# Kernel tuning notes

Measured on AMD Instinct MI355X. Metric: run time of the kernel, lower is better.

Reference implementation:

```python
import jax, jax.numpy as jnp
import numpy as np

N = 512      # state dim n
K = 8        # num_regimes
H = 256      # hidden dim for g0/g1/gate MLPs
B = 8192     # batch
INIT_SCALE = 0.1


def _mlp(x, w1, b1, w2, b2, w3, b3):
    # 2 hidden SiLU layers + linear head (matches ScalarMLP/GateNet with num_layers=2)
    h = jax.nn.silu(x @ w1 + b1)
    h = jax.nn.silu(h @ w2 + b2)
    return h @ w3 + b3


def setup_inputs() -> dict:
    key = jax.random.key(0)
    ks = jax.random.split(key, 12)

    def lin(k, fi, fo):
        kw, kb = jax.random.split(k)
        s = 1.0 / np.sqrt(fi)  # torch nn.Linear default init range
        w = jax.random.uniform(kw, (fi, fo), minval=-s, maxval=s, dtype=jnp.float32)
        b = jax.random.uniform(kb, (fo,), minval=-s, maxval=s, dtype=jnp.float32)
        return w, b

    g0_w1, g0_b1 = lin(ks[0], N, H)
    g0_w2, g0_b2 = lin(ks[1], H, H)
    g0_w3, g0_b3 = lin(ks[2], H, 1)
    g1_w1, g1_b1 = lin(ks[3], N, H)
    g1_w2, g1_b2 = lin(ks[4], H, H)
    g1_w3, g1_b3 = lin(ks[5], H, 1)
    gt_w1, gt_b1 = lin(ks[6], N, H)
    gt_w2, gt_b2 = lin(ks[7], H, H)
    gt_w3, gt_b3 = lin(ks[8], H, K)
    W = jax.random.uniform(ks[9], (K, N, N), minval=-INIT_SCALE, maxval=INIT_SCALE, dtype=jnp.float32)
    z = jax.random.normal(ks[10], (B, 2 * N), dtype=jnp.float32)
    return dict(z=z,
                g0_w1=g0_w1, g0_b1=g0_b1, g0_w2=g0_w2, g0_b2=g0_b2, g0_w3=g0_w3, g0_b3=g0_b3,
                g1_w1=g1_w1, g1_b1=g1_b1, g1_w2=g1_w2, g1_b2=g1_b2, g1_w3=g1_w3, g1_b3=g1_b3,
                gt_w1=gt_w1, gt_b1=gt_b1, gt_w2=gt_w2, gt_b2=gt_b2, gt_w3=gt_w3, gt_b3=gt_b3,
                W=W)


def reference(z,
              g0_w1, g0_b1, g0_w2, g0_b2, g0_w3, g0_b3,
              g1_w1, g1_b1, g1_w2, g1_b2, g1_w3, g1_b3,
              gt_w1, gt_b1, gt_w2, gt_b2, gt_w3, gt_b3,
              W):
    n = W.shape[-1]
    x0, x1 = z[:, :n], z[:, n:]

    def U(x0_, x1_):
        e0 = jnp.sum(_mlp(x0_, g0_w1, g0_b1, g0_w2, g0_b2, g0_w3, g0_b3))  # scalar
        e1 = jnp.sum(_mlp(x1_, g1_w1, g1_b1, g1_w2, g1_b2, g1_w3, g1_b3))
        alpha = jax.nn.softmax(_mlp(x0_, gt_w1, gt_b1, gt_w2, gt_b2, gt_w3, gt_b3), axis=-1)  # [B,K]
        # per-sample per-regime bilinear x1^T W_k x0 -> avoids materializing [B,n,n] W_eff
        q = jnp.einsum('bi,kij,bj->bk', x1_, W, x0_)
        return e0 + e1 + jnp.sum(alpha * q)

    grad_x0, grad_x1 = jax.grad(U, argnums=(0, 1))(x0, x1)
    return jnp.concatenate([-grad_x0, -grad_x1], axis=-1)  # [B, 2n]
```

## Files before the change

kernel.cpp:

```cpp
#include <hip/hip_runtime.h>
#include <cstdint>
#include <cstddef>

constexpr int BTOT = 8192, N = 512, H = 256, K = 8;

typedef __attribute__((ext_vector_type(8))) short short8v;
typedef __attribute__((ext_vector_type(4))) float f32x4;

__device__ __forceinline__ float bf2f(unsigned short u) {
    return __uint_as_float(((uint32_t)u) << 16);
}
__device__ __forceinline__ unsigned short f2bf(float f) {
    uint32_t u = __float_as_uint(f);
    uint32_t r = (u + 0x7FFFu + ((u >> 16) & 1u)) >> 16;
    return (unsigned short)r;
}

typedef __attribute__((address_space(3))) unsigned int lds_uint;
typedef __attribute__((address_space(1))) const unsigned int glob_uint;
__device__ __forceinline__ void async16(const unsigned short* g, unsigned short* l) {
    __builtin_amdgcn_global_load_lds((glob_uint*)g, (lds_uint*)l, 16, 0, 0);
}

struct GArg {
    const unsigned short* A;
    const unsigned short* Bt;
    const float* bias;
    const float* w3v;
    const unsigned short* dmul;
    unsigned short* ob;
    unsigned short* ob2;
    float* of;
    int lda, ldbt, Ka, lddm, ldob, ldof;
};

enum { EPI_BF = 0, EPI_FWD = 1, EPI_BWD2 = 2, EPI_NEG = 3, EPI_NEGW = 4 };

template<int EPI>
__global__ __launch_bounds__(256) void gemm_g(GArg ga0, GArg ga1, GArg ga2)
{
    const int z = blockIdx.z;
    const GArg g = (z == 0) ? ga0 : (z == 1) ? ga1 : ga2;

    __shared__ __attribute__((aligned(16))) unsigned short As[3 * 128 * 32];
    __shared__ __attribute__((aligned(16))) unsigned short Bs[3 * 128 * 32];
    const int tid = threadIdx.x;
    const int lane = tid & 63, wave = tid >> 6;
    const int m0 = blockIdx.y * 128, n0 = blockIdx.x * 128;
    const int wr = (wave >> 1) * 64, wc = (wave & 1) * 64;
    const int rr = lane & 15;
    const int kb = ((lane >> 4) ^ (lane & 3)) << 3;

    const int r0 = tid >> 2;
    const int ko0 = (((tid & 3) ^ (r0 & 3)) << 3);
    const unsigned short* gA0 = g.A + (size_t)(m0 + r0) * g.lda + ko0;
    const unsigned short* gA1 = g.A + (size_t)(m0 + r0 + 64) * g.lda + ko0;
    const unsigned short* gB0 = g.Bt + (size_t)(n0 + r0) * g.ldbt + ko0;
    const unsigned short* gB1 = g.Bt + (size_t)(n0 + r0 + 64) * g.ldbt + ko0;

    auto stage = [&](int t, int buf) {
        const int k0 = t << 5;
        async16(gA0 + k0, As + buf * 4096 + tid * 8);
        async16(gA1 + k0, As + buf * 4096 + (tid + 256) * 8);
        async16(gB0 + k0, Bs + buf * 4096 + tid * 8);
        async16(gB1 + k0, Bs + buf * 4096 + (tid + 256) * 8);
    };

    f32x4 acc[4][4];
    #pragma unroll
    for (int i = 0; i < 4; ++i)
        #pragma unroll
        for (int j = 0; j < 4; ++j) acc[i][j] = (f32x4){0.f, 0.f, 0.f, 0.f};

    const int nt = g.Ka >> 5;

    stage(0, 0);
    if (nt > 1) stage(1, 1);

    int buf = 0;
    for (int t = 0; t < nt; ++t) {
        if (t + 1 < nt) { asm volatile("s_waitcnt vmcnt(4)" ::: "memory"); }
        else            { asm volatile("s_waitcnt vmcnt(0)" ::: "memory"); }
        __builtin_amdgcn_s_barrier();
        if (t + 2 < nt) {
            int b2 = buf + 2; if (b2 >= 3) b2 -= 3;
            stage(t + 2, b2);
        }
        short8v af[4], bfr[4];
        #pragma unroll
        for (int i = 0; i < 4; ++i)
            af[i] = *(const short8v*)(As + buf * 4096 + (wr + i * 16 + rr) * 32 + kb);
        #pragma unroll
        for (int j = 0; j < 4; ++j)
            bfr[j] = *(const short8v*)(Bs + buf * 4096 + (wc + j * 16 + rr) * 32 + kb);
        #pragma unroll
        for (int i = 0; i < 4; ++i)
            #pragma unroll
            for (int j = 0; j < 4; ++j)
                acc[i][j] = __builtin_amdgcn_mfma_f32_16x16x32_bf16(af[i], bfr[j], acc[i][j], 0, 0, 0);
        if (++buf == 3) buf = 0;
    }

    const int orow = (lane >> 4) * 4;
    #pragma unroll
    for (int i = 0; i < 4; ++i) {
        #pragma unroll
        for (int e = 0; e < 4; ++e) {
            const int row = m0 + wr + i * 16 + orow + e;
            #pragma unroll
            for (int j = 0; j < 4; ++j) {
                const int col = n0 + wc + rr + j * 16;
                float v = acc[i][j][e];
                if constexpr (EPI == EPI_BF) {
                    g.ob[(size_t)row * g.ldob + col] = f2bf(v);
                } else if constexpr (EPI == EPI_FWD) {
                    float p = v + g.bias[col];
                    float s = 1.f / (1.f + expf(-p));
                    if (g.ob) g.ob[(size_t)row * g.ldob + col] = f2bf(p * s);
                    float ds = s * (1.f + p * (1.f - s));
                    if (g.w3v) ds *= g.w3v[col];
                    g.ob2[(size_t)row * g.ldob + col] = f2bf(ds);
                } else if constexpr (EPI == EPI_BWD2) {
                    float t = v * bf2f(g.dmul[(size_t)row * g.lddm + col]);
                    g.ob[(size_t)row * g.ldob + col] = f2bf(t);
                } else if constexpr (EPI == EPI_NEG) {
                    g.of[(size_t)row * g.ldof + col] -= v;
                } else {
                    g.of[(size_t)row * g.ldof + col] = -v;
                }
            }
        }
    }
}

struct CvtJob { const float* src; unsigned short* dst; int ls, ld, cols32, tiles, trans; };
struct CvtTable { CvtJob j[12]; };

constexpr int PREP_ZB = BTOT * 1024 / (256 * 4);
constexpr int PREP_TW = (N / 32) * (N / 32) * K;

__global__ __launch_bounds__(256) void k_prep(const float* __restrict__ z,
    unsigned short* __restrict__ Zbf, const float* __restrict__ W,
    unsigned short* __restrict__ Wbf, unsigned short* __restrict__ WTbf,
    CvtTable T)
{
    __shared__ float t[32][33];
    int bid = blockIdx.x;
    if (bid < PREP_ZB) {
        int g = (bid * 256 + threadIdx.x) * 4;
        float4 v = *(const float4*)(z + g);
        ushort4 u;
        u.x = f2bf(v.x); u.y = f2bf(v.y); u.z = f2bf(v.z); u.w = f2bf(v.w);
        *(ushort4*)(Zbf + g) = u;
        return;
    }
    bid -= PREP_ZB;
    int tc = threadIdx.x & 31, tr = threadIdx.x >> 5;
    if (bid < PREP_TW) {
        int k = bid >> 8, rem = bid & 255;
        int i0 = (rem >> 4) * 32, j0 = (rem & 15) * 32;
        const float* Wk = W + (size_t)k * N * N;
        #pragma unroll
        for (int r = 0; r < 32; r += 8) {
            float v = Wk[(size_t)(i0 + tr + r) * N + j0 + tc];
            t[tr + r][tc] = v;
            Wbf[(size_t)k * N * N + (size_t)(i0 + tr + r) * N + j0 + tc] = f2bf(v);
        }
        __syncthreads();
        #pragma unroll
        for (int r = 0; r < 32; r += 8)
            WTbf[(size_t)k * N * N + (size_t)(j0 + tr + r) * N + i0 + tc] = f2bf(t[tc][tr + r]);
        return;
    }
    bid -= PREP_TW;
    int ji = 0;
    while (bid >= T.j[ji].tiles) { bid -= T.j[ji].tiles; ++ji; }
    CvtJob jb = T.j[ji];
    int i0 = (bid / jb.cols32) * 32, c0 = (bid % jb.cols32) * 32;
    if (!jb.trans) {
        #pragma unroll
        for (int r = 0; r < 32; r += 8)
            jb.dst[(size_t)(i0 + tr + r) * jb.ld + c0 + tc] =
                f2bf(jb.src[(size_t)(i0 + tr + r) * jb.ls + c0 + tc]);
    } else {
        #pragma unroll
        for (int r = 0; r < 32; r += 8)
            t[tr + r][tc] = jb.src[(size_t)(i0 + tr + r) * jb.ls + c0 + tc];
        __syncthreads();
        #pragma unroll
        for (int r = 0; r < 32; r += 8)
            jb.dst[(size_t)(c0 + tr + r) * jb.ld + i0 + tc] = f2bf(t[tc][tr + r]);
    }
}

__global__ __launch_bounds__(256) void k_head_s(const unsigned short* __restrict__ h2t,
    const float* __restrict__ w3t, const float* __restrict__ b3t,
    float* __restrict__ s)
{
    int t = threadIdx.x;
    int bl = t >> 3, k = t & 7;
    int b = blockIdx.x * 32 + bl;
    const unsigned short* ar = h2t + (size_t)b * H;
    float acc = b3t[k];
    for (int h0 = 0; h0 < H; h0 += 8) {
        short8v hv = *(const short8v*)(ar + h0);
        #pragma unroll
        for (int u = 0; u < 8; ++u)
            acc += bf2f((unsigned short)hv[u]) * w3t[(h0 + u) * K + k];
    }
    s[b * K + k] = acc;
}

__global__ __launch_bounds__(256) void k_q(const unsigned short* __restrict__ v0,
    const unsigned short* __restrict__ zb, float* __restrict__ q)
{
    int w = threadIdx.x >> 6, lane = threadIdx.x & 63;
    int idx = blockIdx.x * 4 + w;
    int b = idx >> 3, k = idx & 7;
    const unsigned short* vr = v0 + ((size_t)b * K + k) * N;
    const unsigned short* xr = zb + (size_t)b * 1024 + 512;
    short8v vv = *(const short8v*)(vr + lane * 8);
    short8v xv = *(const short8v*)(xr + lane * 8);
    float s = 0.f;
    #pragma unroll
    for (int t = 0; t < 8; ++t)
        s += bf2f((unsigned short)vv[t]) * bf2f((unsigned short)xv[t]);
    for (int off = 32; off; off >>= 1) s += __shfl_down(s, off, 64);
    if (lane == 0) q[idx] = s;
}

__global__ __launch_bounds__(256) void k_d(const float* __restrict__ s,
    const float* __restrict__ q, float* __restrict__ alpha,
    float* __restrict__ dd, int Bc)
{
    int b = blockIdx.x * 256 + threadIdx.x;
    if (b >= Bc) return;
    float sv[K], qv[K];
    float m = -1e30f;
    #pragma unroll
    for (int k = 0; k < K; ++k) { sv[k] = s[b * K + k]; m = fmaxf(m, sv[k]); }
    float sum = 0.f;
    #pragma unroll
    for (int k = 0; k < K; ++k) { sv[k] = expf(sv[k] - m); sum += sv[k]; }
    float inv = 1.f / sum, qbar = 0.f;
    #pragma unroll
    for (int k = 0; k < K; ++k) { sv[k] *= inv; qv[k] = q[b * K + k]; qbar += sv[k] * qv[k]; }
    #pragma unroll
    for (int k = 0; k < K; ++k) {
        alpha[b * K + k] = sv[k];
        dd[b * K + k] = sv[k] * (qv[k] - qbar);
    }
}

__global__ __launch_bounds__(256) void k_u2t(
    const unsigned short* __restrict__ d2_t,
    const float* __restrict__ w3t, const float* __restrict__ dd,
    unsigned short* __restrict__ u2_t)
{
    int g = blockIdx.x * 256 + threadIdx.x;
    int h = g & (H - 1), b = g >> 8;
    float s = 0.f;
    #pragma unroll
    for (int k = 0; k < K; ++k) s += w3t[h * K + k] * dd[b * K + k];
    u2_t[g] = f2bf(s * bf2f(d2_t[g]));
}

__global__ __launch_bounds__(256) void k_gxq2(const unsigned short* __restrict__ v0,
    const unsigned short* __restrict__ v1, const float* __restrict__ alpha,
    float* __restrict__ out)
{
    int g = blockIdx.x * 256 + threadIdx.x;
    int b = g >> 6, jb = (g & 63) << 3;
    float al[K];
    #pragma unroll
    for (int k = 0; k < K; ++k) al[k] = alpha[b * K + k];
    const unsigned short* pv0 = v0 + (size_t)b * K * N + jb;
    const unsigned short* pv1 = v1 + (size_t)b * K * N + jb;
    float s0[8] = {}, s1[8] = {};
    #pragma unroll
    for (int k = 0; k < K; ++k) {
        short8v w1 = *(const short8v*)(pv1 + (size_t)k * N);
        short8v w0 = *(const short8v*)(pv0 + (size_t)k * N);
        #pragma unroll
        for (int t = 0; t < 8; ++t) {
            s0[t] += al[k] * bf2f((unsigned short)w1[t]);
            s1[t] += al[k] * bf2f((unsigned short)w0[t]);
        }
    }
    float* o0 = out + (size_t)b * 1024 + jb;
    float* o1 = o0 + 512;
    float4 x0 = *(float4*)o0, x1 = *(float4*)(o0 + 4);
    x0.x -= s0[0]; x0.y -= s0[1]; x0.z -= s0[2]; x0.w -= s0[3];
    x1.x -= s0[4]; x1.y -= s0[5]; x1.z -= s0[6]; x1.w -= s0[7];
    *(float4*)o0 = x0; *(float4*)(o0 + 4) = x1;
    float4 y0 = *(float4*)o1, y1 = *(float4*)(o1 + 4);
    y0.x -= s1[0]; y0.y -= s1[1]; y0.z -= s1[2]; y0.w -= s1[3];
    y1.x -= s1[4]; y1.y -= s1[5]; y1.z -= s1[6]; y1.w -= s1[7];
    *(float4*)o1 = y0; *(float4*)(o1 + 4) = y1;
}

extern "C" void kernel_launch(void* const* d_in, const int* in_sizes, int n_in,
                              void* d_out, int out_size, void* d_ws, size_t ws_size,
                              hipStream_t stream) {
    const float* z     = (const float*)d_in[0];
    const float* g0_w1 = (const float*)d_in[1];  const float* g0_b1 = (const float*)d_in[2];
    const float* g0_w2 = (const float*)d_in[3];  const float* g0_b2 = (const float*)d_in[4];
    const float* g0_w3 = (const float*)d_in[5];
    const float* g1_w1 = (const float*)d_in[7];  const float* g1_b1 = (const float*)d_in[8];
    const float* g1_w2 = (const float*)d_in[9];  const float* g1_b2 = (const float*)d_in[10];
    const float* g1_w3 = (const float*)d_in[11];
    const float* gt_w1 = (const float*)d_in[13]; const float* gt_b1 = (const float*)d_in[14];
    const float* gt_w2 = (const float*)d_in[15]; const float* gt_b2 = (const float*)d_in[16];
    const float* gt_w3 = (const float*)d_in[17]; const float* gt_b3 = (const float*)d_in[18];
    const float* W     = (const float*)d_in[19];
    float* out = (float*)d_out;

    char* wsb = (char*)d_ws;
    size_t off = 0;
    auto aus = [&](size_t n) -> unsigned short* {
        unsigned short* r = (unsigned short*)(wsb + off);
        off += ((n * 2 + 255) & ~(size_t)255);
        return r;
    };
    auto af4 = [&](size_t n) -> float* {
        float* r = (float*)(wsb + off);
        off += ((n * 4 + 255) & ~(size_t)255);
        return r;
    };

    unsigned short* Zbf  = aus((size_t)BTOT * 1024);
    unsigned short* Wbf  = aus((size_t)K * N * N);
    unsigned short* WTbf = aus((size_t)K * N * N);
    unsigned short* w1T[3], *w2T[3], *w2N[3];
    for (int i = 0; i < 3; ++i) w1T[i] = aus((size_t)H * N);
    for (int i = 0; i < 3; ++i) w2T[i] = aus((size_t)H * H);
    for (int i = 0; i < 3; ++i) w2N[i] = aus((size_t)H * H);
    unsigned short* w1N1  = aus((size_t)N * H);
    unsigned short* w1cat = aus((size_t)N * 2 * H);
    unsigned short* h1[3], *d1b[3], *u2[3];
    for (int i = 0; i < 3; ++i) h1[i]  = aus((size_t)BTOT * H);
    for (int i = 0; i < 3; ++i) d1b[i] = aus((size_t)BTOT * H);
    for (int i = 0; i < 3; ++i) u2[i]  = aus((size_t)BTOT * H);
    unsigned short* d2t   = aus((size_t)BTOT * H);
    unsigned short* h2t   = aus((size_t)BTOT * H);
    unsigned short* t2cat = aus((size_t)BTOT * 512);
    unsigned short* t21   = aus((size_t)BTOT * H);
    float* sbuf = af4((size_t)BTOT * K);
    float* qbuf = af4((size_t)BTOT * K);
    float* abuf = af4((size_t)BTOT * K);
    float* dbuf = af4((size_t)BTOT * K);

    int Bcv = BTOT;
    while (off + 2 * (((size_t)Bcv * K * N * 2 + 255) & ~(size_t)255) > ws_size && Bcv > 128)
        Bcv >>= 1;
    unsigned short* v0 = aus((size_t)Bcv * K * N);
    unsigned short* v1 = aus((size_t)Bcv * K * N);
    const bool full = (Bcv == BTOT);

    const dim3 blk(256);

    if (!full)
        hipMemsetAsync(d_out, 0, (size_t)out_size * sizeof(float), stream);

    CvtTable T;
    int nj = 0, tot = 0;
    auto addjob = [&](const float* src, int ls, unsigned short* dst, int ld,
                      int rows, int cols, int trans) {
        CvtJob jb; jb.src = src; jb.dst = dst; jb.ls = ls; jb.ld = ld;
        jb.cols32 = cols / 32; jb.tiles = (rows / 32) * (cols / 32); jb.trans = trans;
        T.j[nj++] = jb; tot += jb.tiles;
    };
    addjob(g0_w1, H, w1T[0], N, N, H, 1);
    addjob(g1_w1, H, w1T[1], N, N, H, 1);
    addjob(gt_w1, H, w1T[2], N, N, H, 1);
    addjob(g0_w2, H, w2T[0], H, H, H, 1);
    addjob(g1_w2, H, w2T[1], H, H, H, 1);
    addjob(gt_w2, H, w2T[2], H, H, H, 1);
    addjob(g0_w2, H, w2N[0], H, H, H, 0);
    addjob(g1_w2, H, w2N[1], H, H, H, 0);
    addjob(gt_w2, H, w2N[2], H, H, H, 0);
    addjob(g1_w1, H, w1N1, H, N, H, 0);
    addjob(g0_w1, H, w1cat, 2 * H, N, H, 0);
    addjob(gt_w1, H, w1cat + H, 2 * H, N, H, 0);
    k_prep<<<PREP_ZB + PREP_TW + tot, blk, 0, stream>>>(z, Zbf, W, Wbf, WTbf, T);

    auto mk = [](const unsigned short* A, int lda, const unsigned short* Bt, int ldbt, int Ka) {
        GArg g; g.A = A; g.Bt = Bt; g.bias = nullptr; g.w3v = nullptr; g.dmul = nullptr;
        g.ob = nullptr; g.ob2 = nullptr; g.of = nullptr;
        g.lda = lda; g.ldbt = ldbt; g.Ka = Ka; g.lddm = 0; g.ldob = 0; g.ldof = 0;
        return g;
    };

    {
        const float* bs[3] = {g0_b1, g1_b1, gt_b1};
        GArg a[3];
        for (int i = 0; i < 3; ++i) {
            a[i] = mk(Zbf + (i == 1 ? 512 : 0), 1024, w1T[i], N, N);
            a[i].bias = bs[i]; a[i].ob = h1[i]; a[i].ob2 = d1b[i]; a[i].ldob = H;
        }
        gemm_g<EPI_FWD><<<dim3(H / 128, BTOT / 128, 3), blk, 0, stream>>>(a[0], a[1], a[2]);
    }
    {
        const float* bs[3] = {g0_b2, g1_b2, gt_b2};
        const float* w3[3] = {g0_w3, g1_w3, nullptr};
        GArg a[3];
        for (int i = 0; i < 3; ++i) {
            a[i] = mk(h1[i], H, w2T[i], H, H);
            a[i].bias = bs[i];
            a[i].w3v = w3[i];
            a[i].ob  = (i == 2) ? h2t : nullptr;
            a[i].ob2 = (i == 2) ? d2t : u2[i];
            a[i].ldob = H;
        }
        gemm_g<EPI_FWD><<<dim3(H / 128, BTOT / 128, 3), blk, 0, stream>>>(a[0], a[1], a[2]);
    }
    k_head_s<<<BTOT / 32, blk, 0, stream>>>(h2t, gt_w3, gt_b3, sbuf);

    for (int cb = 0; cb < BTOT; cb += Bcv) {
        GArg a[2];
        a[0] = mk(Zbf + (size_t)cb * 1024, 1024, Wbf, N, N);
        a[0].ob = v0; a[0].ldob = K * N;
        a[1] = mk(Zbf + (size_t)cb * 1024 + 512, 1024, WTbf, N, N);
        a[1].ob = v1; a[1].ldob = K * N;
        gemm_g<EPI_BF><<<dim3(K * N / 128, Bcv / 128, 2), blk, 0, stream>>>(a[0], a[1], a[1]);

        k_q<<<Bcv * K / 4, blk, 0, stream>>>(v0, Zbf + (size_t)cb * 1024, qbuf + (size_t)cb * K);
        k_d<<<(Bcv + 255) / 256, blk, 0, stream>>>(sbuf + (size_t)cb * K, qbuf + (size_t)cb * K,
                                                   abuf + (size_t)cb * K, dbuf + (size_t)cb * K, Bcv);
        if (!full)
            k_gxq2<<<Bcv * 64 / 256, blk, 0, stream>>>(v0, v1, abuf + (size_t)cb * K,
                                                       out + (size_t)cb * 1024);
    }

    k_u2t<<<BTOT * H / 256, blk, 0, stream>>>(d2t, gt_w3, dbuf, u2[2]);

    {
        GArg a[3];
        a[0] = mk(u2[0], H, w2N[0], H, H);
        a[0].dmul = d1b[0]; a[0].lddm = H; a[0].ob = t2cat;     a[0].ldob = 512;
        a[1] = mk(u2[1], H, w2N[1], H, H);
        a[1].dmul = d1b[1]; a[1].lddm = H; a[1].ob = t21;       a[1].ldob = H;
        a[2] = mk(u2[2], H, w2N[2], H, H);
        a[2].dmul = d1b[2]; a[2].lddm = H; a[2].ob = t2cat + H; a[2].ldob = 512;
        gemm_g<EPI_BWD2><<<dim3(H / 128, BTOT / 128, 3), blk, 0, stream>>>(a[0], a[1], a[2]);
    }
    {
        GArg a[2];
        a[0] = mk(t2cat, 512, w1cat, 2 * H, 512);
        a[0].of = out;       a[0].ldof = 1024;
        a[1] = mk(t21, H, w1N1, H, H);
        a[1].of = out + 512; a[1].ldof = 1024;
        if (full) {
            gemm_g<EPI_NEGW><<<dim3(N / 128, BTOT / 128, 2), blk, 0, stream>>>(a[0], a[1], a[1]);
            k_gxq2<<<BTOT * 64 / 256, blk, 0, stream>>>(v0, v1, abuf, out);
        } else {
            gemm_g<EPI_NEG><<<dim3(N / 128, BTOT / 128, 2), blk, 0, stream>>>(a[0], a[1], a[1]);
        }
    }
}
```

Measured before the change: 259.5 us.

## Fuse gate head into layer-2 epilogue and merge q/softmax/u2 kernels

Computes the gate logits inside the second-layer GEMM epilogue with shuffle reductions and atomicAdd into a zeroed buffer, so the h2 activation store and the separate head kernel go away. In the full-batch path, the q dot products, softmax/dd and u2 computation are merged into one per-sample kernel, removing three launches and the intermediate q/dd buffers. In exchange the epilogue carries more register pressure and atomics, needs an extra memset, and the bias b3 moves into the softmax step.

```diff
diff --git a/kernel.cpp b/kernel.cpp
--- a/kernel.cpp
+++ b/kernel.cpp
@@ -31,6 +31,8 @@
     unsigned short* ob;
     unsigned short* ob2;
     float* of;
+    float* sout;
+    const float* w3s;
     int lda, ldbt, Ka, lddm, ldob, ldof;
 };
 
@@ -107,26 +109,55 @@
         #pragma unroll
         for (int e = 0; e < 4; ++e) {
             const int row = m0 + wr + i * 16 + orow + e;
-            #pragma unroll
-            for (int j = 0; j < 4; ++j) {
-                const int col = n0 + wc + rr + j * 16;
-                float v = acc[i][j][e];
-                if constexpr (EPI == EPI_BF) {
-                    g.ob[(size_t)row * g.ldob + col] = f2bf(v);
-                } else if constexpr (EPI == EPI_FWD) {
-                    float p = v + g.bias[col];
+            if constexpr (EPI == EPI_FWD) {
+                float sq[K];
+                const bool do_s = (g.sout != nullptr);
+                #pragma unroll
+                for (int kk = 0; kk < K; ++kk) sq[kk] = 0.f;
+                #pragma unroll
+                for (int j = 0; j < 4; ++j) {
+                    const int col = n0 + wc + rr + j * 16;
+                    float p = acc[i][j][e] + g.bias[col];
                     float s = 1.f / (1.f + expf(-p));
                     if (g.ob) g.ob[(size_t)row * g.ldob + col] = f2bf(p * s);
                     float ds = s * (1.f + p * (1.f - s));
                     if (g.w3v) ds *= g.w3v[col];
                     g.ob2[(size_t)row * g.ldob + col] = f2bf(ds);
-                } else if constexpr (EPI == EPI_BWD2) {
-                    float t = v * bf2f(g.dmul[(size_t)row * g.lddm + col]);
-                    g.ob[(size_t)row * g.ldob + col] = f2bf(t);
-                } else if constexpr (EPI == EPI_NEG) {
-                    g.of[(size_t)row * g.ldof + col] -= v;
-                } else {
-                    g.of[(size_t)row * g.ldof + col] = -v;
+                    if (do_s) {
+                        float sl = p * s;
+                        float4 wa = *(const float4*)(g.w3s + (size_t)col * K);
+                        float4 wb = *(const float4*)(g.w3s + (size_t)col * K + 4);
+                        sq[0] += sl * wa.x; sq[1] += sl * wa.y;
+                        sq[2] += sl * wa.z; sq[3] += sl * wa.w;
+                        sq[4] += sl * wb.x; sq[5] += sl * wb.y;
+                        sq[6] += sl * wb.z; sq[7] += sl * wb.w;
+                    }
+                }
+                if (do_s) {
+                    #pragma unroll
+                    for (int m = 1; m < 16; m <<= 1)
+                        #pragma unroll
+                        for (int kk = 0; kk < K; ++kk) sq[kk] += __shfl_xor(sq[kk], m, 64);
+                    if ((lane & 15) == 0)
+                        #pragma unroll
+                        for (int kk = 0; kk < K; ++kk)
+                            atomicAdd(g.sout + (size_t)row * K + kk, sq[kk]);
+                }
+            } else {
+                #pragma unroll
+                for (int j = 0; j < 4; ++j) {
+                    const int col = n0 + wc + rr + j * 16;
+                    float v = acc[i][j][e];
+                    if constexpr (EPI == EPI_BF) {
+                        g.ob[(size_t)row * g.ldob + col] = f2bf(v);
+                    } else if constexpr (EPI == EPI_BWD2) {
+                        float t = v * bf2f(g.dmul[(size_t)row * g.lddm + col]);
+                        g.ob[(size_t)row * g.ldob + col] = f2bf(t);
+                    } else if constexpr (EPI == EPI_NEG) {
+                        g.of[(size_t)row * g.ldof + col] -= v;
+                    } else {
+                        g.of[(size_t)row * g.ldof + col] = -v;
+                    }
                 }
             }
         }
@@ -193,22 +224,56 @@
     }
 }
 
-__global__ __launch_bounds__(256) void k_head_s(const unsigned short* __restrict__ h2t,
-    const float* __restrict__ w3t, const float* __restrict__ b3t,
-    float* __restrict__ s)
-{
-    int t = threadIdx.x;
-    int bl = t >> 3, k = t & 7;
-    int b = blockIdx.x * 32 + bl;
-    const unsigned short* ar = h2t + (size_t)b * H;
-    float acc = b3t[k];
-    for (int h0 = 0; h0 < H; h0 += 8) {
-        short8v hv = *(const short8v*)(ar + h0);
-        #pragma unroll
-        for (int u = 0; u < 8; ++u)
-            acc += bf2f((unsigned short)hv[u]) * w3t[(h0 + u) * K + k];
-    }
-    s[b * K + k] = acc;
+__global__ __launch_bounds__(512) void k_qdu(const unsigned short* __restrict__ v0,
+    const unsigned short* __restrict__ zb, const float* __restrict__ s,
+    const float* __restrict__ b3t, const float* __restrict__ w3t,
+    const unsigned short* __restrict__ d2t,
+    float* __restrict__ alpha, unsigned short* __restrict__ u2_t)
+{
+    __shared__ float qv[K];
+    __shared__ float sal[K], sdd[K];
+    const int b = blockIdx.x;
+    const int tid = threadIdx.x;
+    const int w = tid >> 6, lane = tid & 63;
+
+    {
+        const unsigned short* vr = v0 + ((size_t)b * K + w) * N;
+        const unsigned short* xr = zb + (size_t)b * 1024 + 512;
+        short8v vv = *(const short8v*)(vr + lane * 8);
+        short8v xv = *(const short8v*)(xr + lane * 8);
+        float sq = 0.f;
+        #pragma unroll
+        for (int t = 0; t < 8; ++t)
+            sq += bf2f((unsigned short)vv[t]) * bf2f((unsigned short)xv[t]);
+        for (int off = 32; off; off >>= 1) sq += __shfl_down(sq, off, 64);
+        if (lane == 0) qv[w] = sq;
+    }
+    __syncthreads();
+    if (tid == 0) {
+        float sv[K], qq[K];
+        float m = -1e30f;
+        #pragma unroll
+        for (int k = 0; k < K; ++k) { sv[k] = s[(size_t)b * K + k] + b3t[k]; m = fmaxf(m, sv[k]); }
+        float sum = 0.f;
+        #pragma unroll
+        for (int k = 0; k < K; ++k) { sv[k] = expf(sv[k] - m); sum += sv[k]; }
+        float inv = 1.f / sum, qbar = 0.f;
+        #pragma unroll
+        for (int k = 0; k < K; ++k) { sv[k] *= inv; qq[k] = qv[k]; qbar += sv[k] * qq[k]; }
+        #pragma unroll
+        for (int k = 0; k < K; ++k) {
+            sal[k] = sv[k];
+            sdd[k] = sv[k] * (qq[k] - qbar);
+        }
+    }
+    __syncthreads();
+    if (tid < K) alpha[(size_t)b * K + tid] = sal[tid];
+    if (tid < H) {
+        float acc = 0.f;
+        #pragma unroll
+        for (int k = 0; k < K; ++k) acc += w3t[tid * K + k] * sdd[k];
+        u2_t[(size_t)b * H + tid] = f2bf(acc * bf2f(d2t[(size_t)b * H + tid]));
+    }
 }
 
 __global__ __launch_bounds__(256) void k_q(const unsigned short* __restrict__ v0,
@@ -230,6 +295,7 @@
 }
 
 __global__ __launch_bounds__(256) void k_d(const float* __restrict__ s,
+    const float* __restrict__ b3t,
     const float* __restrict__ q, float* __restrict__ alpha,
     float* __restrict__ dd, int Bc)
 {
@@ -238,7 +304,7 @@
     float sv[K], qv[K];
     float m = -1e30f;
     #pragma unroll
-    for (int k = 0; k < K; ++k) { sv[k] = s[b * K + k]; m = fmaxf(m, sv[k]); }
+    for (int k = 0; k < K; ++k) { sv[k] = s[b * K + k] + b3t[k]; m = fmaxf(m, sv[k]); }
     float sum = 0.f;
     #pragma unroll
     for (int k = 0; k < K; ++k) { sv[k] = expf(sv[k] - m); sum += sv[k]; }
@@ -342,7 +408,6 @@
     for (int i = 0; i < 3; ++i) d1b[i] = aus((size_t)BTOT * H);
     for (int i = 0; i < 3; ++i) u2[i]  = aus((size_t)BTOT * H);
     unsigned short* d2t   = aus((size_t)BTOT * H);
-    unsigned short* h2t   = aus((size_t)BTOT * H);
     unsigned short* t2cat = aus((size_t)BTOT * 512);
     unsigned short* t21   = aus((size_t)BTOT * H);
     float* sbuf = af4((size_t)BTOT * K);
@@ -361,6 +426,7 @@
 
     if (!full)
         hipMemsetAsync(d_out, 0, (size_t)out_size * sizeof(float), stream);
+    hipMemsetAsync(sbuf, 0, (size_t)BTOT * K * sizeof(float), stream);
 
     CvtTable T;
     int nj = 0, tot = 0;
@@ -387,6 +453,7 @@
     auto mk = [](const unsigned short* A, int lda, const unsigned short* Bt, int ldbt, int Ka) {
         GArg g; g.A = A; g.Bt = Bt; g.bias = nullptr; g.w3v = nullptr; g.dmul = nullptr;
         g.ob = nullptr; g.ob2 = nullptr; g.of = nullptr;
+        g.sout = nullptr; g.w3s = nullptr;
         g.lda = lda; g.ldbt = ldbt; g.Ka = Ka; g.lddm = 0; g.ldob = 0; g.ldof = 0;
         return g;
     };
@@ -408,13 +475,13 @@
             a[i] = mk(h1[i], H, w2T[i], H, H);
             a[i].bias = bs[i];
             a[i].w3v = w3[i];
-            a[i].ob  = (i == 2) ? h2t : nullptr;
+            a[i].ob  = nullptr;
             a[i].ob2 = (i == 2) ? d2t : u2[i];
             a[i].ldob = H;
         }
+        a[2].sout = sbuf; a[2].w3s = gt_w3;
         gemm_g<EPI_FWD><<<dim3(H / 128, BTOT / 128, 3), blk, 0, stream>>>(a[0], a[1], a[2]);
     }
-    k_head_s<<<BTOT / 32, blk, 0, stream>>>(h2t, gt_w3, gt_b3, sbuf);
 
     for (int cb = 0; cb < BTOT; cb += Bcv) {
         GArg a[2];
@@ -424,15 +491,20 @@
         a[1].ob = v1; a[1].ldob = K * N;
         gemm_g<EPI_BF><<<dim3(K * N / 128, Bcv / 128, 2), blk, 0, stream>>>(a[0], a[1], a[1]);
 
-        k_q<<<Bcv * K / 4, blk, 0, stream>>>(v0, Zbf + (size_t)cb * 1024, qbuf + (size_t)cb * K);
-        k_d<<<(Bcv + 255) / 256, blk, 0, stream>>>(sbuf + (size_t)cb * K, qbuf + (size_t)cb * K,
-                                                   abuf + (size_t)cb * K, dbuf + (size_t)cb * K, Bcv);
-        if (!full)
+        if (full) {
+            k_qdu<<<BTOT, dim3(512), 0, stream>>>(v0, Zbf, sbuf, gt_b3, gt_w3,
+                                                  d2t, abuf, u2[2]);
+        } else {
+            k_q<<<Bcv * K / 4, blk, 0, stream>>>(v0, Zbf + (size_t)cb * 1024, qbuf + (size_t)cb * K);
+            k_d<<<(Bcv + 255) / 256, blk, 0, stream>>>(sbuf + (size_t)cb * K, gt_b3,
+                                                       qbuf + (size_t)cb * K,
+                                                       abuf + (size_t)cb * K, dbuf + (size_t)cb * K, Bcv);
             k_gxq2<<<Bcv * 64 / 256, blk, 0, stream>>>(v0, v1, abuf + (size_t)cb * K,
                                                        out + (size_t)cb * 1024);
-    }
-
-    k_u2t<<<BTOT * H / 256, blk, 0, stream>>>(d2t, gt_w3, dbuf, u2[2]);
+        }
+    }
+    if (!full)
+        k_u2t<<<BTOT * H / 256, blk, 0, stream>>>(d2t, gt_w3, dbuf, u2[2]);
 
     {
         GArg a[3];
```

Result: slower. 281.0 us (+8.3%).
